# Performance work log

Hardware: AMD Instinct MI355X
Metric: run time of the kernel (lower is better)

The kernel has to match this reference:

```python
import jax, jax.numpy as jnp
import numpy as np
import math

H = 16        # num heads
D = 64        # head dim
HID = 1024    # hidden size
MULT = 2      # GIN MLP multiplier
FRAC = 0.1    # top_k fraction of available predecessors
THR = 0.2     # threshold value
BASE = 10000.0  # rope base
CHUNK = 32    # query-row chunk for max aggregator
NEG = -1e30


def _rope(x, pos):
    # x: (b, H, S, D); pos: (b, S) int
    d = x.shape[-1]
    inv = 1.0 / (BASE ** (jnp.arange(0, d, 2, dtype=jnp.float32) / d))
    ang = pos.astype(jnp.float32)[..., None] * inv            # (b, S, d//2)
    cos = jnp.concatenate([jnp.cos(ang)] * 2, -1)[:, None]    # (b, 1, S, d)
    sin = jnp.concatenate([jnp.sin(ang)] * 2, -1)[:, None]
    x1, x2 = jnp.split(x, 2, axis=-1)
    return x * cos + jnp.concatenate([-x2, x1], -1) * sin


def _scaled_topk_causal(adj):
    # faithful vectorization of scaled_topk_causal_4d: per query row i, keep
    # top max(1, ceil(FRAC*i)) of the (threshold-filtered) strict predecessors.
    S = adj.shape[-1]
    j = jnp.arange(S)
    strict = j[None, :] < j[:, None]                           # (S, S) j < i
    # torch: filtered = a[:, :i] * (a >= thr)  -> below-threshold become 0
    filtered = jnp.where(strict, jnp.where(adj >= THR, adj, 0.0), NEG)
    order = jnp.argsort(-filtered, axis=-1)                    # descending, stable
    rank = jnp.argsort(order, axis=-1)                         # inverse permutation
    k = jnp.maximum(1, jnp.ceil(FRAC * jnp.arange(S, dtype=jnp.float32))).astype(jnp.int32)
    k = k.at[0].set(0)                                         # row 0 has no predecessors
    return ((rank < k[None, None, :, None]) & strict).astype(adj.dtype)


def reference(hidden_states, Wq, Wk, Wv, Wo, W1, W2, eps, position_ids):
    b, S, _ = hidden_states.shape
    q = (hidden_states @ Wq).reshape(b, S, H, D).transpose(0, 2, 1, 3)
    kk = (hidden_states @ Wk).reshape(b, S, H, D).transpose(0, 2, 1, 3)
    v = (hidden_states @ Wv).reshape(b, S, H, D).transpose(0, 2, 1, 3)
    q = _rope(q, position_ids)
    kk = _rope(kk, position_ids)
    scores = jnp.einsum('bhid,bhjd->bhij', q, kk) / math.sqrt(D)
    adj = _scaled_topk_causal(scores)                          # binary (b,H,S,S)
    deg = adj.sum(-1)                                          # (b,H,S)
    denom = jnp.maximum(deg, 1.0)[..., None]
    s_agg = jnp.einsum('bhij,bhjd->bhid', adj, v)              # sum
    m_agg = s_agg / denom                                      # mean
    var = jnp.maximum(jnp.einsum('bhij,bhjd->bhid', adj, v * v) / denom - m_agg ** 2, 0.0)
    # max aggregator: masked max over selected predecessors, chunked over rows
    nc = S // CHUNK
    adj_c = jnp.moveaxis(adj.reshape(b, H, nc, CHUNK, S), 2, 0)  # (nc,b,H,C,S)
    mx = jax.lax.map(
        lambda ac: jnp.max(jnp.where(ac[..., None] > 0, v[:, :, None, :, :], NEG), axis=-2),
        adj_c)                                                 # (nc,b,H,C,D)
    mx = jnp.moveaxis(mx, 0, 2).reshape(b, H, S, D)
    mx = jnp.where(deg[..., None] > 0, mx, 0.0)
    comb = jnp.concatenate([s_agg, m_agg, mx, var], -1)        # (b,H,S,4D)
    h1 = jax.nn.silu(jnp.einsum('bhsf,hfm->bhsm', comb, W1))   # per-head GIN MLP
    head_out = jnp.einsum('bhsm,hmd->bhsd', h1, W2) + eps * v  # epsilon-scaled residual
    return head_out.transpose(0, 2, 1, 3).reshape(b, S, H * D) @ Wo


def setup_inputs() -> dict:
    key = jax.random.key(0)
    ks = jax.random.split(key, 8)
    b, S = 1, 1024
    sc = 0.02
    return {
        'hidden_states': jax.random.normal(ks[0], (b, S, HID), jnp.float32),
        'Wq': jax.random.normal(ks[1], (HID, H * D), jnp.float32) * sc,
        'Wk': jax.random.normal(ks[2], (HID, H * D), jnp.float32) * sc,
        'Wv': jax.random.normal(ks[3], (HID, H * D), jnp.float32) * sc,
        'Wo': jax.random.normal(ks[4], (H * D, HID), jnp.float32) * sc,
        'W1': jax.random.normal(ks[5], (H, 4 * D, MULT * D), jnp.float32) * sc,
        'W2': jax.random.normal(ks[6], (H, MULT * D, D), jnp.float32) * sc,
        'eps': jnp.asarray(0.1, jnp.float32),
        'position_ids': jnp.arange(S, dtype=jnp.int32)[None, :],
    }
```

## Files before the change

kernel.cpp:

```cpp
#include <hip/hip_runtime.h>
#include <math.h>

#define NEGF  -1e30f
#define TAU   1e-6f

static __device__ __forceinline__ int imin(int a, int b) { return a < b ? a : b; }

template <int MODE>
__global__ __launch_bounds__(256) void gemm64(
    const float* __restrict__ A, const float* __restrict__ B, float* __restrict__ C,
    const float* __restrict__ R, const float* __restrict__ eps_p,
    int M, int N, int K, int lda, int ldb, int ldc,
    long sA, long sB, long sC)
{
  const int z = blockIdx.z;
  A += (long)z * sA;
  B += (long)z * sB;
  float* Cf = C + (long)z * sC;
  const float* Rz = (MODE == 2) ? (R + (long)z * sC) : nullptr;

  const int bm = blockIdx.x * 64;
  const int bn = blockIdx.y * 64;
  const int tid = threadIdx.x;
  const int r0 = (tid >> 4) * 4;
  const int c0 = (tid & 15) * 4;

  __shared__ float As[16][68];
  __shared__ float Bs[16][64];

  float acc[4][4] = {};

  const int ar = tid >> 2;
  const int ac = (tid & 3) * 4;
  const int br = tid >> 4;
  const int bc = (tid & 15) * 4;

  for (int kt = 0; kt < K; kt += 16) {
    float4 av = *(const float4*)(A + (long)(bm + ar) * lda + kt + ac);
    float4 bv = *(const float4*)(B + (long)(kt + br) * ldb + bn + bc);
    As[ac + 0][ar] = av.x;
    As[ac + 1][ar] = av.y;
    As[ac + 2][ar] = av.z;
    As[ac + 3][ar] = av.w;
    *(float4*)&Bs[br][bc] = bv;
    __syncthreads();
#pragma unroll
    for (int kk = 0; kk < 16; ++kk) {
      const float4 xa = *(const float4*)&As[kk][r0];
      const float4 yb = *(const float4*)&Bs[kk][c0];
      acc[0][0] += xa.x * yb.x; acc[0][1] += xa.x * yb.y; acc[0][2] += xa.x * yb.z; acc[0][3] += xa.x * yb.w;
      acc[1][0] += xa.y * yb.x; acc[1][1] += xa.y * yb.y; acc[1][2] += xa.y * yb.z; acc[1][3] += xa.y * yb.w;
      acc[2][0] += xa.z * yb.x; acc[2][1] += xa.z * yb.y; acc[2][2] += xa.z * yb.z; acc[2][3] += xa.z * yb.w;
      acc[3][0] += xa.w * yb.x; acc[3][1] += xa.w * yb.y; acc[3][2] += xa.w * yb.z; acc[3][3] += xa.w * yb.w;
    }
    __syncthreads();
  }

  const float ev = (MODE == 2) ? eps_p[0] : 0.0f;
#pragma unroll
  for (int e = 0; e < 4; ++e)
#pragma unroll
    for (int f = 0; f < 4; ++f) {
      const int r = bm + r0 + e;
      const int c = bn + c0 + f;
      float x = acc[e][f];
      if (MODE == 1) x = x / (1.0f + expf(-x));
      if (MODE == 2) x += ev * Rz[(long)r * ldc + c];
      Cf[(long)r * ldc + c] = x;
    }
}

__global__ __launch_bounds__(256) void gemm_qkv(
    const float* __restrict__ A,
    const float* __restrict__ Wq, const float* __restrict__ Wk, const float* __restrict__ Wv,
    float* __restrict__ qo, float* __restrict__ ko, float* __restrict__ vo)
{
  const int z = blockIdx.z;
  const float* B = (z == 0) ? Wq : (z == 1) ? Wk : Wv;
  float* C = (z == 0) ? qo : (z == 1) ? ko : vo;

  const int bm = blockIdx.x * 64;
  const int bn = blockIdx.y * 64;
  const int tid = threadIdx.x;
  const int r0 = (tid >> 4) * 4;
  const int c0 = (tid & 15) * 4;

  __shared__ float As[2][32][68];
  __shared__ float Bs[2][32][64];

  float acc[4][4] = {};
  float tot[4][4] = {};

  const int ar = tid >> 2;
  const int ac = (tid & 3) * 8;
  const int br = tid >> 3;
  const int bc = (tid & 7) * 8;

  {
    float4 a0 = *(const float4*)(A + (long)(bm + ar) * 1024 + ac);
    float4 a1 = *(const float4*)(A + (long)(bm + ar) * 1024 + ac + 4);
    float4 b0 = *(const float4*)(B + (long)br * 1024 + bn + bc);
    float4 b1 = *(const float4*)(B + (long)br * 1024 + bn + bc + 4);
    As[0][ac + 0][ar] = a0.x; As[0][ac + 1][ar] = a0.y;
    As[0][ac + 2][ar] = a0.z; As[0][ac + 3][ar] = a0.w;
    As[0][ac + 4][ar] = a1.x; As[0][ac + 5][ar] = a1.y;
    As[0][ac + 6][ar] = a1.z; As[0][ac + 7][ar] = a1.w;
    *(float4*)&Bs[0][br][bc] = b0;
    *(float4*)&Bs[0][br][bc + 4] = b1;
  }
  __syncthreads();

  int cur = 0;
  for (int kt = 0; kt < 1024; kt += 32) {
    const bool more = (kt + 32 < 1024);
    float4 a0n, a1n, b0n, b1n;
    if (more) {
      a0n = *(const float4*)(A + (long)(bm + ar) * 1024 + kt + 32 + ac);
      a1n = *(const float4*)(A + (long)(bm + ar) * 1024 + kt + 32 + ac + 4);
      b0n = *(const float4*)(B + (long)(kt + 32 + br) * 1024 + bn + bc);
      b1n = *(const float4*)(B + (long)(kt + 32 + br) * 1024 + bn + bc + 4);
    }
    if (kt == 384 || kt == 768) {
#pragma unroll
      for (int e = 0; e < 4; ++e)
#pragma unroll
        for (int f = 0; f < 4; ++f) {
          tot[e][f] = __fadd_rn(tot[e][f], acc[e][f]);
          acc[e][f] = 0.0f;
        }
    }
#pragma unroll
    for (int kk = 0; kk < 32; ++kk) {
      const float4 xa = *(const float4*)&As[cur][kk][r0];
      const float4 yb = *(const float4*)&Bs[cur][kk][c0];
      acc[0][0] += xa.x * yb.x; acc[0][1] += xa.x * yb.y; acc[0][2] += xa.x * yb.z; acc[0][3] += xa.x * yb.w;
      acc[1][0] += xa.y * yb.x; acc[1][1] += xa.y * yb.y; acc[1][2] += xa.y * yb.z; acc[1][3] += xa.y * yb.w;
      acc[2][0] += xa.z * yb.x; acc[2][1] += xa.z * yb.y; acc[2][2] += xa.z * yb.z; acc[2][3] += xa.z * yb.w;
      acc[3][0] += xa.w * yb.x; acc[3][1] += xa.w * yb.y; acc[3][2] += xa.w * yb.z; acc[3][3] += xa.w * yb.w;
    }
    if (more) {
      const int nxt = cur ^ 1;
      As[nxt][ac + 0][ar] = a0n.x; As[nxt][ac + 1][ar] = a0n.y;
      As[nxt][ac + 2][ar] = a0n.z; As[nxt][ac + 3][ar] = a0n.w;
      As[nxt][ac + 4][ar] = a1n.x; As[nxt][ac + 5][ar] = a1n.y;
      As[nxt][ac + 6][ar] = a1n.z; As[nxt][ac + 7][ar] = a1n.w;
      *(float4*)&Bs[nxt][br][bc] = b0n;
      *(float4*)&Bs[nxt][br][bc + 4] = b1n;
      __syncthreads();
      cur = nxt;
    }
  }

#pragma unroll
  for (int e = 0; e < 4; ++e)
#pragma unroll
    for (int f = 0; f < 4; ++f)
      C[(long)(bm + r0 + e) * 1024 + bn + c0 + f] = __fadd_rn(tot[e][f], acc[e][f]);
}

__global__ __launch_bounds__(256) void gemm_out(
    const float* __restrict__ A, const float* __restrict__ B, float* __restrict__ C)
{
  const int bm = blockIdx.x * 32;
  const int bn = blockIdx.y * 64;
  const int tid = threadIdx.x;
  const int r0 = (tid >> 4) * 2;
  const int c0 = (tid & 15) * 4;

  __shared__ float As[2][16][36];
  __shared__ float Bs[2][16][64];

  float acc[2][4] = {};

  const int ar = tid >> 3;
  const int ac = (tid & 7) * 2;
  const int br = tid >> 4;
  const int bc = (tid & 15) * 4;

  {
    float2 av = *(const float2*)(A + (long)(bm + ar) * 1024 + ac);
    float4 bv = *(const float4*)(B + (long)br * 1024 + bn + bc);
    As[0][ac + 0][ar] = av.x;
    As[0][ac + 1][ar] = av.y;
    *(float4*)&Bs[0][br][bc] = bv;
  }
  __syncthreads();

  int cur = 0;
  for (int kt = 0; kt < 1024; kt += 16) {
    const bool more = (kt + 16 < 1024);
    float2 avn;
    float4 bvn;
    if (more) {
      avn = *(const float2*)(A + (long)(bm + ar) * 1024 + kt + 16 + ac);
      bvn = *(const float4*)(B + (long)(kt + 16 + br) * 1024 + bn + bc);
    }
#pragma unroll
    for (int kk = 0; kk < 16; ++kk) {
      const float2 xa = *(const float2*)&As[cur][kk][r0];
      const float4 yb = *(const float4*)&Bs[cur][kk][c0];
      acc[0][0] += xa.x * yb.x; acc[0][1] += xa.x * yb.y; acc[0][2] += xa.x * yb.z; acc[0][3] += xa.x * yb.w;
      acc[1][0] += xa.y * yb.x; acc[1][1] += xa.y * yb.y; acc[1][2] += xa.y * yb.z; acc[1][3] += xa.y * yb.w;
    }
    if (more) {
      const int nxt = cur ^ 1;
      As[nxt][ac + 0][ar] = avn.x;
      As[nxt][ac + 1][ar] = avn.y;
      *(float4*)&Bs[nxt][br][bc] = bvn;
      __syncthreads();
      cur = nxt;
    }
  }

#pragma unroll
  for (int e = 0; e < 2; ++e)
#pragma unroll
    for (int f = 0; f < 4; ++f)
      C[(long)(bm + r0 + e) * 1024 + bn + c0 + f] = acc[e][f];
}

__global__ __launch_bounds__(256) void rope_kernel(float* __restrict__ q,
                                                   float* __restrict__ kb,
                                                   const int* __restrict__ pos_ids)
{
  const int g = blockIdx.x * blockDim.x + threadIdx.x;
  const int t = g & 31;
  const int h = (g >> 5) & 15;
  const int s = (g >> 9) & 1023;
  const int buf = g >> 19;
  float* p = buf ? kb : q;

  const float e = (float)(2 * t) / 64.0f;
  const float p32 = (float)pow(10000.0, (double)e);
  const float inv = __fdiv_rn(1.0f, p32);
  const float posf = (float)pos_ids[s];
  const float ang = __fmul_rn(posf, inv);
  const float c  = (float)cos((double)ang);
  const float sn = (float)sin((double)ang);

  const int base = s * 1024 + h * 64;
  const float x1 = p[base + t];
  const float x2 = p[base + t + 32];
  p[base + t]      = __fadd_rn(__fmul_rn(x1, c), __fmul_rn(-x2, sn));
  p[base + t + 32] = __fadd_rn(__fmul_rn(x2, c), __fmul_rn(x1, sn));
}

__global__ __launch_bounds__(256) void gemm_score(
    const float* __restrict__ q, const float* __restrict__ kb,
    float* __restrict__ S, int headBase)
{
  const int x = blockIdx.x;
  int bmT = 0;
  while ((bmT + 1) * (bmT + 2) / 2 <= x) ++bmT;
  const int bnT = x - bmT * (bmT + 1) / 2;

  const int hl = blockIdx.y;
  const int off = (headBase + hl) * 64;
  const int bm = bmT * 64;
  const int bn = bnT * 64;
  const int tid = threadIdx.x;
  const int r0 = (tid >> 4) * 4;
  const int c0 = (tid & 15) * 4;

  __shared__ float As[16][68];
  __shared__ float Bs[16][68];

  float acc[4][4] = {};

  const int ar = tid >> 2;
  const int ac = (tid & 3) * 4;

  for (int kt = 0; kt < 64; kt += 16) {
    float4 av = *(const float4*)(q  + (long)(bm + ar) * 1024 + off + kt + ac);
    float4 bv = *(const float4*)(kb + (long)(bn + ar) * 1024 + off + kt + ac);
    As[ac + 0][ar] = av.x; As[ac + 1][ar] = av.y;
    As[ac + 2][ar] = av.z; As[ac + 3][ar] = av.w;
    Bs[ac + 0][ar] = bv.x; Bs[ac + 1][ar] = bv.y;
    Bs[ac + 2][ar] = bv.z; Bs[ac + 3][ar] = bv.w;
    __syncthreads();
#pragma unroll
    for (int kk = 0; kk < 16; ++kk) {
      const float4 xa = *(const float4*)&As[kk][r0];
      const float4 yb = *(const float4*)&Bs[kk][c0];
      acc[0][0] += xa.x * yb.x; acc[0][1] += xa.x * yb.y; acc[0][2] += xa.x * yb.z; acc[0][3] += xa.x * yb.w;
      acc[1][0] += xa.y * yb.x; acc[1][1] += xa.y * yb.y; acc[1][2] += xa.y * yb.z; acc[1][3] += xa.y * yb.w;
      acc[2][0] += xa.z * yb.x; acc[2][1] += xa.z * yb.y; acc[2][2] += xa.z * yb.z; acc[2][3] += xa.z * yb.w;
      acc[3][0] += xa.w * yb.x; acc[3][1] += xa.w * yb.y; acc[3][2] += xa.w * yb.z; acc[3][3] += xa.w * yb.w;
    }
    __syncthreads();
  }

#pragma unroll
  for (int e = 0; e < 4; ++e)
#pragma unroll
    for (int f = 0; f < 4; ++f)
      S[((long)hl * 1024 + bm + r0 + e) * 1024 + bn + c0 + f] = acc[e][f] * 0.125f;
}

__global__ __launch_bounds__(256) void select_agg2(
    const float* __restrict__ S, const float* __restrict__ v,
    float* __restrict__ comb, int headBase)
{
  const int i = blockIdx.x;
  const int hl = blockIdx.y;
  const int h = headBase + hl;
  const int tid = threadIdx.x;
  const int lane = tid & 63;
  const int wid = tid >> 6;

  __shared__ int hist[256];
  __shared__ int wtot[4];
  __shared__ int selBinSh, newRkSh, selCntSh;
  __shared__ unsigned vminSh;
  __shared__ int mInIdx;
  __shared__ unsigned WBits;
  __shared__ int outIdxMin;
  __shared__ unsigned long long tbIn, tbOut;
  __shared__ int hypOut, hypIn;
  __shared__ int listLen;
  __shared__ unsigned list[128];
  __shared__ float red[6][4][64];

  if (tid == 0) {
    mInIdx = -1; WBits = 0u; outIdxMin = 0x7FFFFFFF;
    tbIn = ~0ull; tbOut = ~0ull; hypOut = -1; hypIn = -1; listLen = 0;
  }

  const int cs = (i + 255) >> 8;
  const int j0 = tid * cs;
  const int j1 = imin(j0 + cs, i);
  const int nj = (j1 > j0) ? (j1 - j0) : 0;

  float rawr[4];
  unsigned uf[4];
  const float* row = S + ((long)hl * 1024 + i) * 1024;
  for (int m = 0; m < nj; ++m) {
    const float rv = row[j0 + m];
    rawr[m] = rv;
    uf[m] = __float_as_uint((rv >= 0.2f) ? rv : 0.0f);
  }

  const int kk = (i > 0) ? (i + 9) / 10 : 0;
  unsigned V = 0u;
  int need_eq = 0;
  unsigned char f0[4] = {0, 0, 0, 0};

  if (kk > 0) {
    unsigned prefix = 0;
    int rk = kk;
    bool done = false;
    for (int pass = 0; pass < 4; ++pass) {
      const int shift = 24 - 8 * pass;
      hist[tid] = 0;
      __syncthreads();
      for (int m = 0; m < nj; ++m) {
        const unsigned u = uf[m];
        const bool active = (pass == 0) || ((u >> (shift + 8)) == prefix);
        if (active) atomicAdd(&hist[(u >> shift) & 0xFF], 1);
      }
      __syncthreads();
      const int hval = hist[tid];
      int val = hval;
#pragma unroll
      for (int off = 1; off < 64; off <<= 1) {
        int n = __shfl_up(val, off, 64);
        if (lane >= off) val += n;
      }
      if (lane == 63) wtot[wid] = val;
      __syncthreads();
      int wpre = 0;
      for (int w = 0; w < wid; ++w) wpre += wtot[w];
      const int incl = wpre + val;
      const int total = wtot[0] + wtot[1] + wtot[2] + wtot[3];
      const int sfx = total - incl + hval;
      if (sfx >= rk && (sfx - hval) < rk) {
        selBinSh = tid;
        newRkSh = rk - (sfx - hval);
        selCntSh = hval;
      }
      __syncthreads();
      const int selBin = selBinSh;
      prefix = (prefix << 8) | (unsigned)selBin;
      rk = newRkSh;
      const int scnt = selCntSh;
      if (pass == 0 && selBin == 0) {
        V = 0u; need_eq = rk; done = true;
      } else if (rk == scnt) {
        if (tid == 0) vminSh = 0xFFFFFFFFu;
        __syncthreads();
        for (int m = 0; m < nj; ++m)
          if (uf[m] != 0u && (uf[m] >> shift) == prefix) atomicMin(&vminSh, uf[m]);
        __syncthreads();
        V = vminSh; need_eq = 0x3FFFFFFF; done = true;
      }
      if (done) break;
    }
    if (!done) { V = prefix; need_eq = rk; }

    int e = 0;
    for (int m = 0; m < nj; ++m)
      if (uf[m] == V) ++e;
    int val = e;
#pragma unroll
    for (int off = 1; off < 64; off <<= 1) {
      int n = __shfl_up(val, off, 64);
      if (lane >= off) val += n;
    }
    if (lane == 63) wtot[wid] = val;
    __syncthreads();
    int wpre = 0;
    for (int w = 0; w < wid; ++w) wpre += wtot[w];
    int excl = wpre + val - e;
    for (int m = 0; m < nj; ++m) {
      const unsigned u = uf[m];
      if (u > V) f0[m] = 1;
      else if (u == V) { if (excl < need_eq) f0[m] = 1; ++excl; }
    }
  }
  __syncthreads();

  if (kk > 0 && kk < i) {
    unsigned wmax = 0u;
    for (int m = 0; m < nj; ++m) {
      const int j = j0 + m;
      const unsigned u = uf[m];
      if (f0[m]) {
        if (u == V) atomicMax(&mInIdx, j);
        const float fv = __uint_as_float(u);
        const float dd = fv - 0.2f;
        if (fv >= 0.2f && dd < TAU)
          atomicMin(&tbIn, (((unsigned long long)__float_as_uint(dd)) << 32) | (unsigned)j);
      } else {
        wmax = (u > wmax) ? u : wmax;
        if (rawr[m] < 0.2f) {
          const float dd = 0.2f - rawr[m];
          if (dd < TAU)
            atomicMin(&tbOut, (((unsigned long long)__float_as_uint(dd)) << 32) | (unsigned)j);
        }
      }
    }
#pragma unroll
    for (int off = 32; off >= 1; off >>= 1) {
      unsigned o = (unsigned)__shfl_xor((int)wmax, off, 64);
      wmax = (o > wmax) ? o : wmax;
    }
    if (lane == 0) atomicMax(&WBits, wmax);
    __syncthreads();
    for (int m = 0; m < nj; ++m) {
      const int j = j0 + m;
      if (!f0[m] && uf[m] == WBits) atomicMin(&outIdxMin, j);
    }
    __syncthreads();
    if (tid == 0) {
      float bestD = TAU;
      int oI = -1, nI = -1;
      if (outIdxMin != 0x7FFFFFFF && mInIdx >= 0) {
        const float Vf = __uint_as_float(V);
        const float Wf = __uint_as_float(WBits);
        if (!(WBits == V && V == 0u)) {
          const float gapA = Vf - Wf;
          if (gapA < bestD) { bestD = gapA; oI = mInIdx; nI = outIdxMin; }
        }
        if (tbIn != ~0ull) {
          const float d = __uint_as_float((unsigned)(tbIn >> 32));
          const int jj = (int)(tbIn & 0xFFFFFFFFu);
          const bool noop = (WBits == 0u && jj < outIdxMin);
          if (!noop && d < bestD) { bestD = d; oI = jj; nI = outIdxMin; }
        }
        if (tbOut != ~0ull && Vf <= 0.2f) {
          const float d = __uint_as_float((unsigned)(tbOut >> 32));
          const int jj = (int)(tbOut & 0xFFFFFFFFu);
          if (d < bestD) { bestD = d; oI = mInIdx; nI = jj; }
        }
      }
      hypOut = oI; hypIn = nI;
    }
  }
  __syncthreads();

  const bool amb = (hypOut >= 0);
  int cnt = 0;
  unsigned ent[5];
  for (int m = 0; m < nj; ++m) {
    const int j = j0 + m;
    unsigned s1 = f0[m];
    if (amb) { if (j == hypOut) s1 = 0; if (j == hypIn) s1 = 1; }
    if (f0[m] | s1)
      ent[cnt++] = (unsigned)j | ((unsigned)f0[m] << 10) | (s1 << 11);
  }
  int val = cnt;
#pragma unroll
  for (int off = 1; off < 64; off <<= 1) {
    int n = __shfl_up(val, off, 64);
    if (lane >= off) val += n;
  }
  if (lane == 63) wtot[wid] = val;
  __syncthreads();
  int wpre = 0;
  for (int w = 0; w < wid; ++w) wpre += wtot[w];
  const int base = wpre + val - cnt;
  for (int c = 0; c < cnt; ++c) list[base + c] = ent[c];
  if (tid == 0) listLen = wtot[0] + wtot[1] + wtot[2] + wtot[3];
  __syncthreads();

  const int L = listLen;
  float sum0 = 0, sq0 = 0, mx0 = NEGF, sum1 = 0, sq1 = 0, mx1 = NEGF;
  for (int e = wid; e < L; e += 4) {
    const unsigned en = list[e];
    const int j = en & 1023;
    const float vv = v[(long)j * 1024 + h * 64 + lane];
    if (en & (1u << 10)) { sum0 += vv; sq0 += vv * vv; mx0 = fmaxf(mx0, vv); }
    if (en & (1u << 11)) { sum1 += vv; sq1 += vv * vv; mx1 = fmaxf(mx1, vv); }
  }
  red[0][wid][lane] = sum0; red[1][wid][lane] = sq0; red[2][wid][lane] = mx0;
  red[3][wid][lane] = sum1; red[4][wid][lane] = sq1; red[5][wid][lane] = mx1;
  __syncthreads();

  if (tid < 64) {
    float S0 = 0, Q0 = 0, M0 = NEGF, S1 = 0, Q1 = 0, M1 = NEGF;
#pragma unroll
    for (int gg = 0; gg < 4; ++gg) {
      S0 += red[0][gg][tid]; Q0 += red[1][gg][tid]; M0 = fmaxf(M0, red[2][gg][tid]);
      S1 += red[3][gg][tid]; Q1 += red[4][gg][tid]; M1 = fmaxf(M1, red[5][gg][tid]);
    }
    const float denom = (float)(kk > 0 ? kk : 1);
    const float mean0 = S0 / denom, mean1 = S1 / denom;
    const float var0 = fmaxf(Q0 / denom - mean0 * mean0, 0.0f);
    const float var1 = fmaxf(Q1 / denom - mean1 * mean1, 0.0f);
    const float mx0o = (kk > 0) ? M0 : 0.0f;
    const float mx1o = (kk > 0) ? M1 : 0.0f;
    float* crow = comb + ((long)(h * 1024 + i)) * 256;
    crow[tid]       = 0.5f * (S0 + S1);
    crow[64 + tid]  = 0.5f * (mean0 + mean1);
    crow[128 + tid] = 0.5f * (mx0o + mx1o);
    crow[192 + tid] = 0.5f * (var0 + var1);
  }
}

extern "C" void kernel_launch(void* const* d_in, const int* in_sizes, int n_in,
                              void* d_out, int out_size, void* d_ws, size_t ws_size,
                              hipStream_t stream)
{
  const float* hidden = (const float*)d_in[0];
  const float* Wq = (const float*)d_in[1];
  const float* Wk = (const float*)d_in[2];
  const float* Wv = (const float*)d_in[3];
  const float* Wo = (const float*)d_in[4];
  const float* W1 = (const float*)d_in[5];
  const float* W2 = (const float*)d_in[6];
  const float* eps = (const float*)d_in[7];
  const int* pos = (const int*)d_in[8];

  const size_t MB = 1024UL * 1024UL;
  int G = 4;
  if (ws_size >= 28 * MB + 64 * MB) G = 16;
  else if (ws_size >= 28 * MB + 32 * MB) G = 8;

  float* q      = (float*)d_ws;
  float* kbuf   = q + (1 << 20);
  float* v      = kbuf + (1 << 20);
  float* comb   = v + (1 << 20);
  float* scores = comb + (1 << 22);
  float* h1     = scores;
  float* ho     = scores + (1 << 21);

  const dim3 blk(256);

  gemm_qkv<<<dim3(16, 16, 3), blk, 0, stream>>>(hidden, Wq, Wk, Wv, q, kbuf, v);

  rope_kernel<<<4096, blk, 0, stream>>>(q, kbuf, pos);

  for (int g = 0; g < 16; g += G) {
    gemm_score<<<dim3(136, G), blk, 0, stream>>>(q, kbuf, scores, g);
    select_agg2<<<dim3(1024, G), blk, 0, stream>>>(scores, v, comb, g);
  }

  gemm64<1><<<dim3(16, 2, 16), blk, 0, stream>>>(comb, W1, h1, nullptr, nullptr,
      1024, 128, 256, 256, 128, 128, (long)1024 * 256, (long)256 * 128, (long)1024 * 128);

  gemm64<2><<<dim3(16, 1, 16), blk, 0, stream>>>(h1, W2, ho, v, eps,
      1024, 64, 128, 128, 64, 1024, (long)1024 * 128, (long)128 * 64, 64);

  gemm_out<<<dim3(32, 16), blk, 0, stream>>>(ho, Wo, (float*)d_out);
}
```

Measured before the change: 397.4 us.

## Split-K output GEMM, precompute RoPE table, unroll select loops to fixed width

```diff
diff --git a/kernel.cpp b/kernel.cpp
--- a/kernel.cpp
+++ b/kernel.cpp
@@ -5,6 +5,20 @@
 #define TAU   1e-6f
 
 static __device__ __forceinline__ int imin(int a, int b) { return a < b ? a : b; }
+
+static __device__ __forceinline__ void fma44(float A[4][4], const float4 xa, const float4 yb) {
+  A[0][0] += xa.x * yb.x; A[0][1] += xa.x * yb.y; A[0][2] += xa.x * yb.z; A[0][3] += xa.x * yb.w;
+  A[1][0] += xa.y * yb.x; A[1][1] += xa.y * yb.y; A[1][2] += xa.y * yb.z; A[1][3] += xa.y * yb.w;
+  A[2][0] += xa.z * yb.x; A[2][1] += xa.z * yb.y; A[2][2] += xa.z * yb.z; A[2][3] += xa.z * yb.w;
+  A[3][0] += xa.w * yb.x; A[3][1] += xa.w * yb.y; A[3][2] += xa.w * yb.z; A[3][3] += xa.w * yb.w;
+}
+
+static __device__ __forceinline__ void fold44(float T[4][4], float A[4][4]) {
+#pragma unroll
+  for (int e = 0; e < 4; ++e)
+#pragma unroll
+    for (int f = 0; f < 4; ++f) { T[e][f] = __fadd_rn(T[e][f], A[e][f]); A[e][f] = 0.0f; }
+}
 
 template <int MODE>
 __global__ __launch_bounds__(256) void gemm64(
@@ -48,10 +62,7 @@
     for (int kk = 0; kk < 16; ++kk) {
       const float4 xa = *(const float4*)&As[kk][r0];
       const float4 yb = *(const float4*)&Bs[kk][c0];
-      acc[0][0] += xa.x * yb.x; acc[0][1] += xa.x * yb.y; acc[0][2] += xa.x * yb.z; acc[0][3] += xa.x * yb.w;
-      acc[1][0] += xa.y * yb.x; acc[1][1] += xa.y * yb.y; acc[1][2] += xa.y * yb.z; acc[1][3] += xa.y * yb.w;
-      acc[2][0] += xa.z * yb.x; acc[2][1] += xa.z * yb.y; acc[2][2] += xa.z * yb.z; acc[2][3] += xa.z * yb.w;
-      acc[3][0] += xa.w * yb.x; acc[3][1] += xa.w * yb.y; acc[3][2] += xa.w * yb.z; acc[3][3] += xa.w * yb.w;
+      fma44(acc, xa, yb);
     }
     __syncthreads();
   }
@@ -70,7 +81,7 @@
     }
 }
 
-__global__ __launch_bounds__(256) void gemm_qkv(
+__global__ __launch_bounds__(256) void gemm_qkv64(
     const float* __restrict__ A,
     const float* __restrict__ Wq, const float* __restrict__ Wk, const float* __restrict__ Wv,
     float* __restrict__ qo, float* __restrict__ ko, float* __restrict__ vo)
@@ -121,22 +132,13 @@
       b1n = *(const float4*)(B + (long)(kt + 32 + br) * 1024 + bn + bc + 4);
     }
     if (kt == 384 || kt == 768) {
-#pragma unroll
-      for (int e = 0; e < 4; ++e)
-#pragma unroll
-        for (int f = 0; f < 4; ++f) {
-          tot[e][f] = __fadd_rn(tot[e][f], acc[e][f]);
-          acc[e][f] = 0.0f;
-        }
+      fold44(tot, acc);
     }
 #pragma unroll
     for (int kk = 0; kk < 32; ++kk) {
       const float4 xa = *(const float4*)&As[cur][kk][r0];
       const float4 yb = *(const float4*)&Bs[cur][kk][c0];
-      acc[0][0] += xa.x * yb.x; acc[0][1] += xa.x * yb.y; acc[0][2] += xa.x * yb.z; acc[0][3] += xa.x * yb.w;
-      acc[1][0] += xa.y * yb.x; acc[1][1] += xa.y * yb.y; acc[1][2] += xa.y * yb.z; acc[1][3] += xa.y * yb.w;
-      acc[2][0] += xa.z * yb.x; acc[2][1] += xa.z * yb.y; acc[2][2] += xa.z * yb.z; acc[2][3] += xa.z * yb.w;
-      acc[3][0] += xa.w * yb.x; acc[3][1] += xa.w * yb.y; acc[3][2] += xa.w * yb.z; acc[3][3] += xa.w * yb.w;
+      fma44(acc, xa, yb);
     }
     if (more) {
       const int nxt = cur ^ 1;
@@ -158,70 +160,38 @@
       C[(long)(bm + r0 + e) * 1024 + bn + c0 + f] = __fadd_rn(tot[e][f], acc[e][f]);
 }
 
-__global__ __launch_bounds__(256) void gemm_out(
-    const float* __restrict__ A, const float* __restrict__ B, float* __restrict__ C)
-{
-  const int bm = blockIdx.x * 32;
-  const int bn = blockIdx.y * 64;
-  const int tid = threadIdx.x;
-  const int r0 = (tid >> 4) * 2;
-  const int c0 = (tid & 15) * 4;
-
-  __shared__ float As[2][16][36];
-  __shared__ float Bs[2][16][64];
-
-  float acc[2][4] = {};
-
-  const int ar = tid >> 3;
-  const int ac = (tid & 7) * 2;
-  const int br = tid >> 4;
-  const int bc = (tid & 15) * 4;
-
-  {
-    float2 av = *(const float2*)(A + (long)(bm + ar) * 1024 + ac);
-    float4 bv = *(const float4*)(B + (long)br * 1024 + bn + bc);
-    As[0][ac + 0][ar] = av.x;
-    As[0][ac + 1][ar] = av.y;
-    *(float4*)&Bs[0][br][bc] = bv;
-  }
-  __syncthreads();
-
-  int cur = 0;
-  for (int kt = 0; kt < 1024; kt += 16) {
-    const bool more = (kt + 16 < 1024);
-    float2 avn;
-    float4 bvn;
-    if (more) {
-      avn = *(const float2*)(A + (long)(bm + ar) * 1024 + kt + 16 + ac);
-      bvn = *(const float4*)(B + (long)(kt + 16 + br) * 1024 + bn + bc);
-    }
-#pragma unroll
-    for (int kk = 0; kk < 16; ++kk) {
-      const float2 xa = *(const float2*)&As[cur][kk][r0];
-      const float4 yb = *(const float4*)&Bs[cur][kk][c0];
-      acc[0][0] += xa.x * yb.x; acc[0][1] += xa.x * yb.y; acc[0][2] += xa.x * yb.z; acc[0][3] += xa.x * yb.w;
-      acc[1][0] += xa.y * yb.x; acc[1][1] += xa.y * yb.y; acc[1][2] += xa.y * yb.z; acc[1][3] += xa.y * yb.w;
-    }
-    if (more) {
-      const int nxt = cur ^ 1;
-      As[nxt][ac + 0][ar] = avn.x;
-      As[nxt][ac + 1][ar] = avn.y;
-      *(float4*)&Bs[nxt][br][bc] = bvn;
-      __syncthreads();
-      cur = nxt;
-    }
-  }
-
-#pragma unroll
-  for (int e = 0; e < 2; ++e)
-#pragma unroll
-    for (int f = 0; f < 4; ++f)
-      C[(long)(bm + r0 + e) * 1024 + bn + c0 + f] = acc[e][f];
-}
-
-__global__ __launch_bounds__(256) void rope_kernel(float* __restrict__ q,
-                                                   float* __restrict__ kb,
-                                                   const int* __restrict__ pos_ids)
+__global__ __launch_bounds__(256) void combine_out(
+    const float4* __restrict__ p, float4* __restrict__ dst)
+{
+  const int idx = blockIdx.x * 256 + threadIdx.x;
+  const float4 a = p[idx];
+  const float4 b = p[idx + (1 << 18)];
+  float4 r;
+  r.x = __fadd_rn(a.x, b.x);
+  r.y = __fadd_rn(a.y, b.y);
+  r.z = __fadd_rn(a.z, b.z);
+  r.w = __fadd_rn(a.w, b.w);
+  dst[idx] = r;
+}
+
+__global__ __launch_bounds__(256) void rope_table(
+    const int* __restrict__ pos_ids, float2* __restrict__ tab)
+{
+  const int g = blockIdx.x * 256 + threadIdx.x;
+  const int t = g & 31;
+  const int s = g >> 5;
+
+  const float e = (float)(2 * t) / 64.0f;
+  const float p32 = (float)pow(10000.0, (double)e);
+  const float inv = __fdiv_rn(1.0f, p32);
+  const float posf = (float)pos_ids[s];
+  const float ang = __fmul_rn(posf, inv);
+  tab[g] = make_float2((float)cos((double)ang), (float)sin((double)ang));
+}
+
+__global__ __launch_bounds__(256) void rope_apply(float* __restrict__ q,
+                                                  float* __restrict__ kb,
+                                                  const float2* __restrict__ tab)
 {
   const int g = blockIdx.x * blockDim.x + threadIdx.x;
   const int t = g & 31;
@@ -230,13 +200,9 @@
   const int buf = g >> 19;
   float* p = buf ? kb : q;
 
-  const float e = (float)(2 * t) / 64.0f;
-  const float p32 = (float)pow(10000.0, (double)e);
-  const float inv = __fdiv_rn(1.0f, p32);
-  const float posf = (float)pos_ids[s];
-  const float ang = __fmul_rn(posf, inv);
-  const float c  = (float)cos((double)ang);
-  const float sn = (float)sin((double)ang);
+  const float2 cs = tab[s * 32 + t];
+  const float c  = cs.x;
+  const float sn = cs.y;
 
   const int base = s * 1024 + h * 64;
   const float x1 = p[base + t];
@@ -282,10 +248,7 @@
     for (int kk = 0; kk < 16; ++kk) {
       const float4 xa = *(const float4*)&As[kk][r0];
       const float4 yb = *(const float4*)&Bs[kk][c0];
-      acc[0][0] += xa.x * yb.x; acc[0][1] += xa.x * yb.y; acc[0][2] += xa.x * yb.z; acc[0][3] += xa.x * yb.w;
-      acc[1][0] += xa.y * yb.x; acc[1][1] += xa.y * yb.y; acc[1][2] += xa.y * yb.z; acc[1][3] += xa.y * yb.w;
-      acc[2][0] += xa.z * yb.x; acc[2][1] += xa.z * yb.y; acc[2][2] += xa.z * yb.z; acc[2][3] += xa.z * yb.w;
-      acc[3][0] += xa.w * yb.x; acc[3][1] += xa.w * yb.y; acc[3][2] += xa.w * yb.z; acc[3][3] += xa.w * yb.w;
+      fma44(acc, xa, yb);
     }
     __syncthreads();
   }
@@ -334,29 +297,42 @@
   float rawr[4];
   unsigned uf[4];
   const float* row = S + ((long)hl * 1024 + i) * 1024;
-  for (int m = 0; m < nj; ++m) {
-    const float rv = row[j0 + m];
+#pragma unroll
+  for (int m = 0; m < 4; ++m) {
+    const float rv = (m < nj) ? row[j0 + m] : 0.0f;
     rawr[m] = rv;
-    uf[m] = __float_as_uint((rv >= 0.2f) ? rv : 0.0f);
+    uf[m] = (m < nj) ? __float_as_uint((rv >= 0.2f) ? rv : 0.0f) : 0u;
   }
 
   const int kk = (i > 0) ? (i + 9) / 10 : 0;
   unsigned V = 0u;
   int need_eq = 0;
-  unsigned char f0[4] = {0, 0, 0, 0};
+  int f0[4] = {0, 0, 0, 0};
 
   if (kk > 0) {
     unsigned prefix = 0;
     int rk = kk;
     bool done = false;
-    for (int pass = 0; pass < 4; ++pass) {
+    for (int pass = 0; pass < 4 && !done; ++pass) {
       const int shift = 24 - 8 * pass;
       hist[tid] = 0;
       __syncthreads();
-      for (int m = 0; m < nj; ++m) {
-        const unsigned u = uf[m];
-        const bool active = (pass == 0) || ((u >> (shift + 8)) == prefix);
-        if (active) atomicAdd(&hist[(u >> shift) & 0xFF], 1);
+      if (pass == 0) {
+        int zc = 0;
+#pragma unroll
+        for (int m = 0; m < 4; ++m) if (m < nj) {
+          const unsigned u = uf[m];
+          if (u) atomicAdd(&hist[u >> 24], 1); else ++zc;
+        }
+#pragma unroll
+        for (int off = 32; off >= 1; off >>= 1) zc += __shfl_xor(zc, off, 64);
+        if (lane == 0 && zc) atomicAdd(&hist[0], zc);
+      } else {
+#pragma unroll
+        for (int m = 0; m < 4; ++m) if (m < nj) {
+          const unsigned u = uf[m];
+          if (u != 0u && (u >> (shift + 8)) == prefix) atomicAdd(&hist[(u >> shift) & 0xFF], 1);
+        }
       }
       __syncthreads();
       const int hval = hist[tid];
@@ -388,18 +364,20 @@
       } else if (rk == scnt) {
         if (tid == 0) vminSh = 0xFFFFFFFFu;
         __syncthreads();
-        for (int m = 0; m < nj; ++m)
-          if (uf[m] != 0u && (uf[m] >> shift) == prefix) atomicMin(&vminSh, uf[m]);
+#pragma unroll
+        for (int m = 0; m < 4; ++m) if (m < nj) {
+          const unsigned u = uf[m];
+          if (u != 0u && (u >> shift) == prefix) atomicMin(&vminSh, u);
+        }
         __syncthreads();
         V = vminSh; need_eq = 0x3FFFFFFF; done = true;
       }
-      if (done) break;
     }
     if (!done) { V = prefix; need_eq = rk; }
 
     int e = 0;
-    for (int m = 0; m < nj; ++m)
-      if (uf[m] == V) ++e;
+#pragma unroll
+    for (int m = 0; m < 4; ++m) if (m < nj) { if (uf[m] == V) ++e; }
     int val = e;
 #pragma unroll
     for (int off = 1; off < 64; off <<= 1) {
@@ -411,7 +389,8 @@
     int wpre = 0;
     for (int w = 0; w < wid; ++w) wpre += wtot[w];
     int excl = wpre + val - e;
-    for (int m = 0; m < nj; ++m) {
+#pragma unroll
+    for (int m = 0; m < 4; ++m) if (m < nj) {
       const unsigned u = uf[m];
       if (u > V) f0[m] = 1;
       else if (u == V) { if (excl < need_eq) f0[m] = 1; ++excl; }
@@ -421,7 +400,8 @@
 
   if (kk > 0 && kk < i) {
     unsigned wmax = 0u;
-    for (int m = 0; m < nj; ++m) {
+#pragma unroll
+    for (int m = 0; m < 4; ++m) if (m < nj) {
       const int j = j0 + m;
       const unsigned u = uf[m];
       if (f0[m]) {
@@ -446,7 +426,8 @@
     }
     if (lane == 0) atomicMax(&WBits, wmax);
     __syncthreads();
-    for (int m = 0; m < nj; ++m) {
+#pragma unroll
+    for (int m = 0; m < 4; ++m) if (m < nj) {
       const int j = j0 + m;
       if (!f0[m] && uf[m] == WBits) atomicMin(&outIdxMin, j);
     }
@@ -480,33 +461,43 @@
 
   const bool amb = (hypOut >= 0);
   int cnt = 0;
-  unsigned ent[5];
-  for (int m = 0; m < nj; ++m) {
+#pragma unroll
+  for (int m = 0; m < 4; ++m) if (m < nj) {
     const int j = j0 + m;
-    unsigned s1 = f0[m];
+    int s1 = f0[m];
     if (amb) { if (j == hypOut) s1 = 0; if (j == hypIn) s1 = 1; }
-    if (f0[m] | s1)
-      ent[cnt++] = (unsigned)j | ((unsigned)f0[m] << 10) | (s1 << 11);
-  }
-  int val = cnt;
-#pragma unroll
-  for (int off = 1; off < 64; off <<= 1) {
-    int n = __shfl_up(val, off, 64);
-    if (lane >= off) val += n;
-  }
-  if (lane == 63) wtot[wid] = val;
-  __syncthreads();
-  int wpre = 0;
-  for (int w = 0; w < wid; ++w) wpre += wtot[w];
-  const int base = wpre + val - cnt;
-  for (int c = 0; c < cnt; ++c) list[base + c] = ent[c];
-  if (tid == 0) listLen = wtot[0] + wtot[1] + wtot[2] + wtot[3];
+    if (f0[m] | s1) ++cnt;
+  }
+  {
+    int val = cnt;
+#pragma unroll
+    for (int off = 1; off < 64; off <<= 1) {
+      int n = __shfl_up(val, off, 64);
+      if (lane >= off) val += n;
+    }
+    if (lane == 63) wtot[wid] = val;
+    __syncthreads();
+    int wpre = 0;
+    for (int w = 0; w < wid; ++w) wpre += wtot[w];
+    int base = wpre + val - cnt;
+#pragma unroll
+    for (int m = 0; m < 4; ++m) if (m < nj) {
+      const int j = j0 + m;
+      int s1 = f0[m];
+      if (amb) { if (j == hypOut) s1 = 0; if (j == hypIn) s1 = 1; }
+      if (f0[m] | s1) {
+        list[base] = (unsigned)j | ((unsigned)f0[m] << 10) | ((unsigned)s1 << 11);
+        ++base;
+      }
+    }
+    if (tid == 0) listLen = wtot[0] + wtot[1] + wtot[2] + wtot[3];
+  }
   __syncthreads();
 
   const int L = listLen;
   float sum0 = 0, sq0 = 0, mx0 = NEGF, sum1 = 0, sq1 = 0, mx1 = NEGF;
-  for (int e = wid; e < L; e += 4) {
-    const unsigned en = list[e];
+  for (int e2 = wid; e2 < L; e2 += 4) {
+    const unsigned en = list[e2];
     const int j = en & 1023;
     const float vv = v[(long)j * 1024 + h * 64 + lane];
     if (en & (1u << 10)) { sum0 += vv; sq0 += vv * vv; mx0 = fmaxf(mx0, vv); }
@@ -563,12 +554,15 @@
   float* scores = comb + (1 << 22);
   float* h1     = scores;
   float* ho     = scores + (1 << 21);
+  float2* tab   = (float2*)comb;
+  float* parts  = comb;
 
   const dim3 blk(256);
 
-  gemm_qkv<<<dim3(16, 16, 3), blk, 0, stream>>>(hidden, Wq, Wk, Wv, q, kbuf, v);
-
-  rope_kernel<<<4096, blk, 0, stream>>>(q, kbuf, pos);
+  gemm_qkv64<<<dim3(16, 16, 3), blk, 0, stream>>>(hidden, Wq, Wk, Wv, q, kbuf, v);
+
+  rope_table<<<128, blk, 0, stream>>>(pos, tab);
+  rope_apply<<<4096, blk, 0, stream>>>(q, kbuf, tab);
 
   for (int g = 0; g < 16; g += G) {
     gemm_score<<<dim3(136, G), blk, 0, stream>>>(q, kbuf, scores, g);
@@ -581,5 +575,7 @@
   gemm64<2><<<dim3(16, 1, 16), blk, 0, stream>>>(h1, W2, ho, v, eps,
       1024, 64, 128, 128, 64, 1024, (long)1024 * 128, (long)128 * 64, 64);
 
-  gemm_out<<<dim3(32, 16), blk, 0, stream>>>(ho, Wo, (float*)d_out);
-}
+  gemm64<0><<<dim3(16, 16, 2), blk, 0, stream>>>(ho, Wo, parts, nullptr, nullptr,
+      1024, 1024, 512, 1024, 1024, 1024, 512, (long)512 * 1024, (long)1 << 20);
+  combine_out<<<dim3(1024), blk, 0, stream>>>((const float4*)parts, (float4*)d_out);
+}
```

Result: faster. 382.5 us (-3.8%).
